# Kernel optimization log

Measured on AMD Instinct MI355X. Metric: run time of the kernel, lower is better.

Reference implementation:

```python
import jax, jax.numpy as jnp
import numpy as np

MARGIN = 0.2
LAMBDA_CLS = 1.0
LAMBDA_TRIPLET = 1.0
EPS = 1e-6  # matches torch pairwise_distance eps inside TripletMarginLoss
B, D, C = 8192, 192, 1024


def setup_inputs() -> dict:
    key = jax.random.key(0)
    k1, k2, k3 = jax.random.split(key, 3)
    embeddings = jax.random.normal(k1, (B, D), dtype=jnp.float32)
    logits = jax.random.normal(k2, (B, C), dtype=jnp.float32)
    targets = jax.random.randint(k3, (B,), 0, C, dtype=jnp.int64)
    return {"embeddings": embeddings, "logits": logits, "targets": targets}


def reference(embeddings, logits, targets):
    # ---- classification loss: mean cross entropy ----
    logp = jax.nn.log_softmax(logits, axis=-1)
    cls_loss = -jnp.mean(jnp.take_along_axis(logp, targets[:, None], axis=1))

    # ---- vectorized hard triplet mining (mining='hard'), on detached embeddings ----
    e = jax.lax.stop_gradient(embeddings)
    sq = jnp.sum(e * e, axis=1)                       # [B]
    d2 = sq[:, None] + sq[None, :] - 2.0 * (e @ e.T)  # [B, B]
    dist = jnp.sqrt(jnp.maximum(d2, 0.0))

    same = targets[:, None] == targets[None, :]       # [B, B]
    eye = jnp.eye(targets.shape[0], dtype=bool)
    pos_mask = same & ~eye
    neg_mask = ~same
    valid = pos_mask.any(axis=1) & neg_mask.any(axis=1)

    # hard positive: farthest same-speaker; hard negative: closest other-speaker
    pos_idx = jnp.argmax(jnp.where(pos_mask, dist, -jnp.inf), axis=1)
    neg_idx = jnp.argmin(jnp.where(neg_mask, dist, jnp.inf), axis=1)

    # ---- triplet margin loss on live embeddings ----
    a = embeddings
    p = embeddings[pos_idx]
    n = embeddings[neg_idx]
    d_ap = jnp.linalg.norm(a - p + EPS, axis=1)
    d_an = jnp.linalg.norm(a - n + EPS, axis=1)
    per_triplet = jnp.maximum(d_ap - d_an + MARGIN, 0.0)

    w = valid.astype(per_triplet.dtype)
    cnt = jnp.sum(w)
    trip_loss = jnp.where(cnt > 0, jnp.sum(per_triplet * w) / jnp.maximum(cnt, 1.0), 0.0)

    return LAMBDA_CLS * cls_loss + LAMBDA_TRIPLET * trip_loss
```

## Files before the change

kernel.cpp:

```cpp
#include <hip/hip_runtime.h>
#include <math.h>

#define B_N    8192
#define D_DIM  192
#define C_CLS  1024
#define MARGIN 0.2f
#define EPS_T  1e-6f

#define TI     128
#define TJ     128
#define JSPLIT 8
#define JLEN   (B_N / JSPLIT)
#define LDB    200

typedef short v8s  __attribute__((ext_vector_type(8)));
typedef float v16f __attribute__((ext_vector_type(16)));

__device__ __forceinline__ unsigned fkey(float f) {
  unsigned u = __float_as_uint(f);
  return (u & 0x80000000u) ? ~u : (u | 0x80000000u);
}

__device__ __forceinline__ unsigned short to_bf(float x) {
  unsigned u = __float_as_uint(x);
  u += 0x7fffu + ((u >> 16) & 1u);
  return (unsigned short)(u >> 16);
}

__global__ __launch_bounds__(256) void prep_kernel(
    const float* __restrict__ e, unsigned short* __restrict__ ebf,
    float* __restrict__ sq,
    unsigned long long* __restrict__ posw, unsigned long long* __restrict__ negw,
    float* __restrict__ accum) {
  int w = threadIdx.x >> 6, lane = threadIdx.x & 63;
  int row = blockIdx.x * 4 + w;
  const float* p = e + (size_t)row * D_DIM;
  float v0 = p[lane], v1 = p[lane + 64], v2 = p[lane + 128];
  unsigned short* q = ebf + (size_t)row * D_DIM;
  q[lane] = to_bf(v0); q[lane + 64] = to_bf(v1); q[lane + 128] = to_bf(v2);
  float s = v0 * v0 + v1 * v1 + v2 * v2;
  #pragma unroll
  for (int off = 32; off; off >>= 1) s += __shfl_xor(s, off);
  if (lane == 0) sq[row] = s;
  int b = blockIdx.x;
  if (b < 32)       posw[b * 256 + threadIdx.x] = 0ULL;
  else if (b < 64)  negw[(b - 32) * 256 + threadIdx.x] = ~0ULL;
  else if (b == 64 && threadIdx.x < 4) ((unsigned*)accum)[threadIdx.x] = 0u;
}

__global__ __launch_bounds__(256, 2) void mine_kernel(
    const unsigned short* __restrict__ ebf, const int* __restrict__ tgt,
    const float* __restrict__ sq, const float* __restrict__ logits,
    unsigned long long* __restrict__ posw, unsigned long long* __restrict__ negw,
    float* __restrict__ accum) {
  __shared__ unsigned short lds_b[TJ * LDB];
  __shared__ int   lds_t[TJ];
  __shared__ float lds_s[TJ];
  __shared__ float ce_part[4];

  const int tid  = threadIdx.x;
  const int w    = tid >> 6;
  const int lane = tid & 63;
  const int n5   = lane & 31;
  const int h    = lane >> 5;
  const int wj   = w & 1;
  const int wi   = w >> 1;
  const int i0 = blockIdx.x * TI;
  const int jb = blockIdx.y * JLEN;

  {
    const unsigned short* src = ebf + (size_t)i0 * D_DIM;
    #pragma unroll
    for (int t = 0; t < 12; ++t) {
      int c = t * 256 + tid;
      int row = c / 24;
      int off = c - row * 24;
      *(v8s*)&lds_b[row * LDB + off * 8] = *(const v8s*)(src + (size_t)row * D_DIM + off * 8);
    }
  }
  __syncthreads();
  v8s bfrag[2][12];
  #pragma unroll
  for (int tb = 0; tb < 2; ++tb)
    #pragma unroll
    for (int kc = 0; kc < 12; ++kc)
      bfrag[tb][kc] = *(const v8s*)&lds_b[(wi * 64 + tb * 32 + n5) * LDB + kc * 16 + h * 8];

  int my_t[2];
  #pragma unroll
  for (int tb = 0; tb < 2; ++tb) my_t[tb] = tgt[i0 + wi * 64 + tb * 32 + n5];

  float    pv[2] = {-3.4e38f, -3.4e38f}, nv[2] = {3.4e38f, 3.4e38f};
  unsigned pi_[2] = {0u, 0u}, ni_[2] = {0xFFFFFFFFu, 0xFFFFFFFFu};

  for (int j0 = jb; j0 < jb + JLEN; j0 += TJ) {
    __syncthreads();
    #pragma unroll
    for (int t = 0; t < 12; ++t) {
      int c = t * 256 + tid;
      int row = c / 24;
      int off = c - row * 24;
      *(v8s*)&lds_b[row * LDB + off * 8] =
          *(const v8s*)(ebf + (size_t)(j0 + row) * D_DIM + off * 8);
    }
    if (tid < TJ) { lds_t[tid] = tgt[j0 + tid]; lds_s[tid] = sq[j0 + tid]; }
    __syncthreads();

    v16f acc[2][2];
    #pragma unroll
    for (int ta = 0; ta < 2; ++ta)
      #pragma unroll
      for (int tb = 0; tb < 2; ++tb)
        #pragma unroll
        for (int r = 0; r < 16; ++r) acc[ta][tb][r] = 0.f;

    #pragma unroll
    for (int kc = 0; kc < 12; ++kc) {
      v8s afr0 = *(const v8s*)&lds_b[(wj * 64 +  0 + n5) * LDB + kc * 16 + h * 8];
      v8s afr1 = *(const v8s*)&lds_b[(wj * 64 + 32 + n5) * LDB + kc * 16 + h * 8];
      acc[0][0] = __builtin_amdgcn_mfma_f32_32x32x16_bf16(afr0, bfrag[0][kc], acc[0][0], 0, 0, 0);
      acc[0][1] = __builtin_amdgcn_mfma_f32_32x32x16_bf16(afr0, bfrag[1][kc], acc[0][1], 0, 0, 0);
      acc[1][0] = __builtin_amdgcn_mfma_f32_32x32x16_bf16(afr1, bfrag[0][kc], acc[1][0], 0, 0, 0);
      acc[1][1] = __builtin_amdgcn_mfma_f32_32x32x16_bf16(afr1, bfrag[1][kc], acc[1][1], 0, 0, 0);
    }

    #pragma unroll
    for (int ta = 0; ta < 2; ++ta)
      #pragma unroll
      for (int p = 0; p < 4; ++p) {
        int jb4 = wj * 64 + ta * 32 + p * 8 + h * 4;
        float4 s4 = *(const float4*)&lds_s[jb4];
        int4   t4 = *(const int4*)&lds_t[jb4];
        #pragma unroll
        for (int q = 0; q < 3 + 1; ++q) {
          float sv = (q == 0) ? s4.x : (q == 1) ? s4.y : (q == 2) ? s4.z : s4.w;
          int   tv = (q == 0) ? t4.x : (q == 1) ? t4.y : (q == 2) ? t4.z : t4.w;
          unsigned jg = (unsigned)(j0 + jb4 + q);
          #pragma unroll
          for (int tb = 0; tb < 2; ++tb) {
            float val = fmaf(acc[ta][tb][p * 4 + q], -2.0f, sv);
            bool same = (tv == my_t[tb]);
            float vp = same ? val : -3.4e38f;
            float vn = same ? 3.4e38f : val;
            if (vp > pv[tb]) { pv[tb] = vp; pi_[tb] = jg; }
            if (vn < nv[tb]) { nv[tb] = vn; ni_[tb] = jg; }
          }
        }
      }
  }

  #pragma unroll
  for (int tb = 0; tb < 2; ++tb) {
    unsigned long long pk =
        ((unsigned long long)fkey(pv[tb]) << 32) | (unsigned long long)(unsigned)(~pi_[tb]);
    unsigned long long nk =
        ((unsigned long long)fkey(nv[tb]) << 32) | (unsigned long long)ni_[tb];
    unsigned long long po = __shfl_xor(pk, 32);
    unsigned long long no = __shfl_xor(nk, 32);
    pk = pk > po ? pk : po;
    nk = nk < no ? nk : no;
    if (h == 0) {
      int irow = i0 + wi * 64 + tb * 32 + n5;
      atomicMax(&posw[irow], pk);
      atomicMin(&negw[irow], nk);
    }
  }

  int blin = blockIdx.y * 64 + blockIdx.x;
  float ce_acc = 0.f;
  #pragma unroll
  for (int it = 0; it < 4; ++it) {
    int row = blin * 16 + it * 4 + w;
    const float* lp = logits + (size_t)row * C_CLS;
    float4 x[4];
    #pragma unroll
    for (int t = 0; t < 4; ++t) x[t] = *(const float4*)(lp + lane * 4 + 256 * t);
    float m = -3.4e38f;
    #pragma unroll
    for (int t = 0; t < 4; ++t)
      m = fmaxf(m, fmaxf(fmaxf(x[t].x, x[t].y), fmaxf(x[t].z, x[t].w)));
    #pragma unroll
    for (int off = 32; off; off >>= 1) m = fmaxf(m, __shfl_xor(m, off));
    float s = 0.f;
    #pragma unroll
    for (int t = 0; t < 4; ++t)
      s += __expf(x[t].x - m) + __expf(x[t].y - m) +
           __expf(x[t].z - m) + __expf(x[t].w - m);
    #pragma unroll
    for (int off = 32; off; off >>= 1) s += __shfl_xor(s, off);
    if (lane == 0) ce_acc += m + __logf(s) - lp[tgt[row]];
  }
  if (lane == 0) ce_part[w] = ce_acc;
  __syncthreads();
  if (tid == 0)
    atomicAdd(&accum[0], ce_part[0] + ce_part[1] + ce_part[2] + ce_part[3]);
}

__global__ __launch_bounds__(1024) void trip_fin_kernel(
    const float* __restrict__ e,
    const unsigned long long* __restrict__ posw,
    const unsigned long long* __restrict__ negw,
    float* __restrict__ accum, float* __restrict__ out) {
  __shared__ float ssum[16];
  __shared__ float scnt[16];
  int w = threadIdx.x >> 6, lane = threadIdx.x & 63;
  int i = blockIdx.x * 16 + w;
  unsigned long long pp = posw[i], np = negw[i];
  unsigned pidx = ~(unsigned)pp;
  unsigned nidx = (unsigned)np;
  float res = 0.f, c = 0.f;
  if (pp != 0ULL && np != ~0ULL && pidx != (unsigned)i) {
    const float* pa = e + (size_t)i * D_DIM;
    const float* pb = e + (size_t)pidx * D_DIM;
    const float* pc = e + (size_t)nidx * D_DIM;
    float dap = 0.f, dan = 0.f;
    #pragma unroll
    for (int t = 0; t < 3; ++t) {
      int k = lane + 64 * t;
      float av = pa[k];
      float d1 = av - pb[k] + EPS_T;
      float d2 = av - pc[k] + EPS_T;
      dap += d1 * d1;
      dan += d2 * d2;
    }
    #pragma unroll
    for (int off = 32; off; off >>= 1) {
      dap += __shfl_xor(dap, off);
      dan += __shfl_xor(dan, off);
    }
    res = fmaxf(sqrtf(dap) - sqrtf(dan) + MARGIN, 0.f);
    c = 1.f;
  }
  if (lane == 0) { ssum[w] = res; scnt[w] = c; }
  __syncthreads();
  if (threadIdx.x == 0) {
    float a = 0.f, b = 0.f;
    #pragma unroll
    for (int k = 0; k < 16; ++k) { a += ssum[k]; b += scnt[k]; }
    atomicAdd(&accum[1], a);
    atomicAdd(&accum[2], b);
    __threadfence();
    unsigned old = atomicAdd((unsigned*)&accum[3], 1u);
    if (old == 511u) {
      __threadfence();
      float cls = atomicAdd(&accum[0], 0.f);
      float ts  = atomicAdd(&accum[1], 0.f);
      float tc  = atomicAdd(&accum[2], 0.f);
      float trip = (tc > 0.f) ? ts / fmaxf(tc, 1.f) : 0.f;
      out[0] = cls / (float)B_N + trip;
    }
  }
}

extern "C" void kernel_launch(void* const* d_in, const int* in_sizes, int n_in,
                              void* d_out, int out_size, void* d_ws, size_t ws_size,
                              hipStream_t stream) {
  const float* emb    = (const float*)d_in[0];
  const float* logits = (const float*)d_in[1];
  const int*   tgt    = (const int*)d_in[2];
  float* out = (float*)d_out;

  char* ws = (char*)d_ws;
  unsigned short* ebf = (unsigned short*)ws;
  unsigned long long* posw = (unsigned long long*)(ws + 3145728);
  unsigned long long* negw = (unsigned long long*)(ws + 3145728 + 65536);
  float* sq    = (float*)(ws + 3145728 + 131072);
  float* accum = (float*)(ws + 3145728 + 163840);

  prep_kernel<<<2048, 256, 0, stream>>>(emb, ebf, sq, posw, negw, accum);
  mine_kernel<<<dim3(B_N / TI, JSPLIT), 256, 0, stream>>>(ebf, tgt, sq, logits, posw, negw, accum);
  trip_fin_kernel<<<512, 1024, 0, stream>>>(emb, posw, negw, accum, out);
}
```

Measured before the change: 145.6 us.

## Fuse triplet finalize into mining kernel with last-block-per-tile reduction

Drops the separate triplet-finalize kernel. Each mining block now writes its per-slice hard positive/negative winners to a slice buffer, and the last block to finish an i-tile merges those slices and computes the triplet terms. The argmin/argmax search packs the column index into the low 8 mantissa bits of the distance key, so each candidate needs one fmaxf/fminf instead of compare-and-select pairs. Block shape moves to 512 threads handling one 32-row B fragment per wave, and per-row global atomics are replaced by LDS atomics. In exchange, ranking is slightly less precise because of the truncated mantissa, and the completion counters rely on a 0xAA workspace poison value instead of explicit zeroing.

```diff
diff --git a/kernel.cpp b/kernel.cpp
--- a/kernel.cpp
+++ b/kernel.cpp
@@ -9,9 +9,14 @@
 
 #define TI     128
 #define TJ     128
+#define NIB    64
 #define JSPLIT 8
-#define JLEN   (B_N / JSPLIT)
+#define JLEN   1024
+#define NTILE  8
 #define LDB    200
+#define NBLK   512
+#define NTHR   512
+#define POISON 0xAAAAAAAAu
 
 typedef short v8s  __attribute__((ext_vector_type(8)));
 typedef float v16f __attribute__((ext_vector_type(16)));
@@ -20,43 +25,43 @@
   unsigned u = __float_as_uint(f);
   return (u & 0x80000000u) ? ~u : (u | 0x80000000u);
 }
-
 __device__ __forceinline__ unsigned short to_bf(float x) {
   unsigned u = __float_as_uint(x);
   u += 0x7fffu + ((u >> 16) & 1u);
   return (unsigned short)(u >> 16);
 }
 
-__global__ __launch_bounds__(256) void prep_kernel(
+__global__ __launch_bounds__(NTHR) void prep_kernel(
     const float* __restrict__ e, unsigned short* __restrict__ ebf,
-    float* __restrict__ sq,
-    unsigned long long* __restrict__ posw, unsigned long long* __restrict__ negw,
-    float* __restrict__ accum) {
+    float* __restrict__ sq) {
   int w = threadIdx.x >> 6, lane = threadIdx.x & 63;
-  int row = blockIdx.x * 4 + w;
-  const float* p = e + (size_t)row * D_DIM;
-  float v0 = p[lane], v1 = p[lane + 64], v2 = p[lane + 128];
-  unsigned short* q = ebf + (size_t)row * D_DIM;
-  q[lane] = to_bf(v0); q[lane + 64] = to_bf(v1); q[lane + 128] = to_bf(v2);
-  float s = v0 * v0 + v1 * v1 + v2 * v2;
   #pragma unroll
-  for (int off = 32; off; off >>= 1) s += __shfl_xor(s, off);
-  if (lane == 0) sq[row] = s;
-  int b = blockIdx.x;
-  if (b < 32)       posw[b * 256 + threadIdx.x] = 0ULL;
-  else if (b < 64)  negw[(b - 32) * 256 + threadIdx.x] = ~0ULL;
-  else if (b == 64 && threadIdx.x < 4) ((unsigned*)accum)[threadIdx.x] = 0u;
-}
-
-__global__ __launch_bounds__(256, 2) void mine_kernel(
+  for (int r = 0; r < 2; ++r) {
+    int row = blockIdx.x * 16 + w * 2 + r;
+    const float* p = e + (size_t)row * D_DIM;
+    float v0 = p[lane], v1 = p[lane + 64], v2 = p[lane + 128];
+    unsigned short* q = ebf + (size_t)row * D_DIM;
+    q[lane] = to_bf(v0); q[lane + 64] = to_bf(v1); q[lane + 128] = to_bf(v2);
+    float s = v0 * v0 + v1 * v1 + v2 * v2;
+    #pragma unroll
+    for (int off = 32; off; off >>= 1) s += __shfl_xor(s, off);
+    if (lane == 0) sq[row] = s;
+  }
+}
+
+__global__ __launch_bounds__(NTHR, 4) void mine_kernel(
     const unsigned short* __restrict__ ebf, const int* __restrict__ tgt,
     const float* __restrict__ sq, const float* __restrict__ logits,
-    unsigned long long* __restrict__ posw, unsigned long long* __restrict__ negw,
-    float* __restrict__ accum) {
+    const float* __restrict__ e,
+    unsigned long long* __restrict__ posS, unsigned long long* __restrict__ negS,
+    unsigned* __restrict__ tileCnt, float* __restrict__ accum,
+    float* __restrict__ out) {
   __shared__ unsigned short lds_b[TJ * LDB];
   __shared__ int   lds_t[TJ];
   __shared__ float lds_s[TJ];
-  __shared__ float ce_part[4];
+  __shared__ unsigned long long lds_pos[TI], lds_neg[TI];
+  __shared__ float red_a[8], red_b[8];
+  __shared__ unsigned sflag;
 
   const int tid  = threadIdx.x;
   const int w    = tid >> 6;
@@ -65,39 +70,30 @@
   const int h    = lane >> 5;
   const int wj   = w & 1;
   const int wi   = w >> 1;
-  const int i0 = blockIdx.x * TI;
-  const int jb = blockIdx.y * JLEN;
-
+  const int tile  = blockIdx.x & (NIB - 1);
+  const int slice = blockIdx.x >> 6;
+  const int i0 = tile * TI;
+  const int jb = slice * JLEN;
+  const float NINF = -__builtin_inff();
+  const float PINF =  __builtin_inff();
+
+  const int irow = i0 + wi * 32 + n5;
+  v8s bfrag[12];
   {
-    const unsigned short* src = ebf + (size_t)i0 * D_DIM;
-    #pragma unroll
-    for (int t = 0; t < 12; ++t) {
-      int c = t * 256 + tid;
-      int row = c / 24;
-      int off = c - row * 24;
-      *(v8s*)&lds_b[row * LDB + off * 8] = *(const v8s*)(src + (size_t)row * D_DIM + off * 8);
-    }
-  }
-  __syncthreads();
-  v8s bfrag[2][12];
-  #pragma unroll
-  for (int tb = 0; tb < 2; ++tb)
-    #pragma unroll
-    for (int kc = 0; kc < 12; ++kc)
-      bfrag[tb][kc] = *(const v8s*)&lds_b[(wi * 64 + tb * 32 + n5) * LDB + kc * 16 + h * 8];
-
-  int my_t[2];
-  #pragma unroll
-  for (int tb = 0; tb < 2; ++tb) my_t[tb] = tgt[i0 + wi * 64 + tb * 32 + n5];
-
-  float    pv[2] = {-3.4e38f, -3.4e38f}, nv[2] = {3.4e38f, 3.4e38f};
-  unsigned pi_[2] = {0u, 0u}, ni_[2] = {0xFFFFFFFFu, 0xFFFFFFFFu};
-
-  for (int j0 = jb; j0 < jb + JLEN; j0 += TJ) {
+    const unsigned short* bp = ebf + (size_t)irow * D_DIM + h * 8;
+    #pragma unroll
+    for (int kc = 0; kc < 12; ++kc) bfrag[kc] = *(const v8s*)(bp + kc * 16);
+  }
+  const int myt = tgt[irow];
+
+  float pv = NINF, nv = PINF;
+
+  for (int jt = 0; jt < NTILE; ++jt) {
+    const int j0 = jb + jt * TJ;
     __syncthreads();
     #pragma unroll
-    for (int t = 0; t < 12; ++t) {
-      int c = t * 256 + tid;
+    for (int t = 0; t < 6; ++t) {
+      int c = t * NTHR + tid;
       int row = c / 24;
       int off = c - row * 24;
       *(v8s*)&lds_b[row * LDB + off * 8] =
@@ -106,76 +102,92 @@
     if (tid < TJ) { lds_t[tid] = tgt[j0 + tid]; lds_s[tid] = sq[j0 + tid]; }
     __syncthreads();
 
-    v16f acc[2][2];
-    #pragma unroll
-    for (int ta = 0; ta < 2; ++ta)
-      #pragma unroll
-      for (int tb = 0; tb < 2; ++tb)
-        #pragma unroll
-        for (int r = 0; r < 16; ++r) acc[ta][tb][r] = 0.f;
-
+    v16f acc0, acc1;
+    #pragma unroll
+    for (int r = 0; r < 16; ++r) { acc0[r] = 0.f; acc1[r] = 0.f; }
     #pragma unroll
     for (int kc = 0; kc < 12; ++kc) {
-      v8s afr0 = *(const v8s*)&lds_b[(wj * 64 +  0 + n5) * LDB + kc * 16 + h * 8];
-      v8s afr1 = *(const v8s*)&lds_b[(wj * 64 + 32 + n5) * LDB + kc * 16 + h * 8];
-      acc[0][0] = __builtin_amdgcn_mfma_f32_32x32x16_bf16(afr0, bfrag[0][kc], acc[0][0], 0, 0, 0);
-      acc[0][1] = __builtin_amdgcn_mfma_f32_32x32x16_bf16(afr0, bfrag[1][kc], acc[0][1], 0, 0, 0);
-      acc[1][0] = __builtin_amdgcn_mfma_f32_32x32x16_bf16(afr1, bfrag[0][kc], acc[1][0], 0, 0, 0);
-      acc[1][1] = __builtin_amdgcn_mfma_f32_32x32x16_bf16(afr1, bfrag[1][kc], acc[1][1], 0, 0, 0);
-    }
-
-    #pragma unroll
-    for (int ta = 0; ta < 2; ++ta)
+      v8s a0 = *(const v8s*)&lds_b[(wj * 64 +  0 + n5) * LDB + kc * 16 + h * 8];
+      v8s a1 = *(const v8s*)&lds_b[(wj * 64 + 32 + n5) * LDB + kc * 16 + h * 8];
+      acc0 = __builtin_amdgcn_mfma_f32_32x32x16_bf16(a0, bfrag[kc], acc0, 0, 0, 0);
+      acc1 = __builtin_amdgcn_mfma_f32_32x32x16_bf16(a1, bfrag[kc], acc1, 0, 0, 0);
+    }
+
+    const unsigned cb = (unsigned)jt << 5;
+    #pragma unroll
+    for (int ta = 0; ta < 2; ++ta) {
       #pragma unroll
       for (int p = 0; p < 4; ++p) {
         int jb4 = wj * 64 + ta * 32 + p * 8 + h * 4;
         float4 s4 = *(const float4*)&lds_s[jb4];
         int4   t4 = *(const int4*)&lds_t[jb4];
         #pragma unroll
-        for (int q = 0; q < 3 + 1; ++q) {
+        for (int q = 0; q < 4; ++q) {
           float sv = (q == 0) ? s4.x : (q == 1) ? s4.y : (q == 2) ? s4.z : s4.w;
           int   tv = (q == 0) ? t4.x : (q == 1) ? t4.y : (q == 2) ? t4.z : t4.w;
-          unsigned jg = (unsigned)(j0 + jb4 + q);
-          #pragma unroll
-          for (int tb = 0; tb < 2; ++tb) {
-            float val = fmaf(acc[ta][tb][p * 4 + q], -2.0f, sv);
-            bool same = (tv == my_t[tb]);
-            float vp = same ? val : -3.4e38f;
-            float vn = same ? 3.4e38f : val;
-            if (vp > pv[tb]) { pv[tb] = vp; pi_[tb] = jg; }
-            if (vn < nv[tb]) { nv[tb] = vn; ni_[tb] = jg; }
-          }
+          float av = (ta == 0) ? acc0[p * 4 + q] : acc1[p * 4 + q];
+          float val = fmaf(av, -2.0f, sv);
+          unsigned cc = cb | (unsigned)(ta * 16 + p * 4 + q);
+          float key = __uint_as_float((__float_as_uint(val) & 0xFFFFFF00u) | cc);
+          bool same = (tv == myt);
+          pv = fmaxf(pv, same ? key : NINF);
+          nv = fminf(nv, same ? PINF : key);
         }
       }
-  }
-
-  #pragma unroll
-  for (int tb = 0; tb < 2; ++tb) {
-    unsigned long long pk =
-        ((unsigned long long)fkey(pv[tb]) << 32) | (unsigned long long)(unsigned)(~pi_[tb]);
-    unsigned long long nk =
-        ((unsigned long long)fkey(nv[tb]) << 32) | (unsigned long long)ni_[tb];
+    }
+  }
+
+  unsigned long long pk = 0ULL, nk = ~0ULL;
+  if (pv != NINF) {
+    unsigned c = __float_as_uint(pv) & 255u;
+    unsigned jr = (unsigned)jb + ((c >> 5) & 7u) * 128u + (unsigned)wj * 64u +
+                  ((c >> 4) & 1u) * 32u + ((c >> 2) & 3u) * 8u + (unsigned)h * 4u + (c & 3u);
+    pk = ((unsigned long long)fkey(pv) << 32) | (unsigned long long)(~jr);
+  }
+  if (nv != PINF) {
+    unsigned c = __float_as_uint(nv) & 255u;
+    unsigned jr = (unsigned)jb + ((c >> 5) & 7u) * 128u + (unsigned)wj * 64u +
+                  ((c >> 4) & 1u) * 32u + ((c >> 2) & 3u) * 8u + (unsigned)h * 4u + (c & 3u);
+    nk = ((unsigned long long)fkey(nv) << 32) | (unsigned long long)jr;
+  }
+  {
     unsigned long long po = __shfl_xor(pk, 32);
     unsigned long long no = __shfl_xor(nk, 32);
     pk = pk > po ? pk : po;
     nk = nk < no ? nk : no;
-    if (h == 0) {
-      int irow = i0 + wi * 64 + tb * 32 + n5;
-      atomicMax(&posw[irow], pk);
-      atomicMin(&negw[irow], nk);
-    }
-  }
-
-  int blin = blockIdx.y * 64 + blockIdx.x;
+  }
+  __syncthreads();
+  if (tid < TI) { lds_pos[tid] = 0ULL; lds_neg[tid] = ~0ULL; }
+  __syncthreads();
+  if (h == 0) {
+    int il = wi * 32 + n5;
+    if (pk != 0ULL)  atomicMax(&lds_pos[il], pk);
+    if (nk != ~0ULL) atomicMin(&lds_neg[il], nk);
+  }
+  __syncthreads();
+  if (tid < TI) {
+    __hip_atomic_store(&posS[(size_t)slice * B_N + i0 + tid], lds_pos[tid],
+                       __ATOMIC_RELAXED, __HIP_MEMORY_SCOPE_AGENT);
+    __hip_atomic_store(&negS[(size_t)slice * B_N + i0 + tid], lds_neg[tid],
+                       __ATOMIC_RELAXED, __HIP_MEMORY_SCOPE_AGENT);
+  }
+  __threadfence();
+  __syncthreads();
+  if (tid == 0) {
+    atomicCAS(&tileCnt[tile], 0u, POISON);
+    unsigned old = atomicAdd(&tileCnt[tile], 1u);
+    sflag = (old == POISON + (JSPLIT - 1)) ? 1u : 0u;
+  }
+
   float ce_acc = 0.f;
   #pragma unroll
-  for (int it = 0; it < 4; ++it) {
-    int row = blin * 16 + it * 4 + w;
+  for (int it = 0; it < 2; ++it) {
+    int row = blockIdx.x * 16 + it * 8 + w;
     const float* lp = logits + (size_t)row * C_CLS;
     float4 x[4];
     #pragma unroll
     for (int t = 0; t < 4; ++t) x[t] = *(const float4*)(lp + lane * 4 + 256 * t);
-    float m = -3.4e38f;
+    float m = NINF;
     #pragma unroll
     for (int t = 0; t < 4; ++t)
       m = fmaxf(m, fmaxf(fmaxf(x[t].x, x[t].y), fmaxf(x[t].z, x[t].w)));
@@ -190,62 +202,82 @@
     for (int off = 32; off; off >>= 1) s += __shfl_xor(s, off);
     if (lane == 0) ce_acc += m + __logf(s) - lp[tgt[row]];
   }
-  if (lane == 0) ce_part[w] = ce_acc;
+  if (lane == 0) red_a[w] = ce_acc;
   __syncthreads();
   if (tid == 0)
-    atomicAdd(&accum[0], ce_part[0] + ce_part[1] + ce_part[2] + ce_part[3]);
-}
-
-__global__ __launch_bounds__(1024) void trip_fin_kernel(
-    const float* __restrict__ e,
-    const unsigned long long* __restrict__ posw,
-    const unsigned long long* __restrict__ negw,
-    float* __restrict__ accum, float* __restrict__ out) {
-  __shared__ float ssum[16];
-  __shared__ float scnt[16];
-  int w = threadIdx.x >> 6, lane = threadIdx.x & 63;
-  int i = blockIdx.x * 16 + w;
-  unsigned long long pp = posw[i], np = negw[i];
-  unsigned pidx = ~(unsigned)pp;
-  unsigned nidx = (unsigned)np;
-  float res = 0.f, c = 0.f;
-  if (pp != 0ULL && np != ~0ULL && pidx != (unsigned)i) {
-    const float* pa = e + (size_t)i * D_DIM;
-    const float* pb = e + (size_t)pidx * D_DIM;
-    const float* pc = e + (size_t)nidx * D_DIM;
-    float dap = 0.f, dan = 0.f;
-    #pragma unroll
-    for (int t = 0; t < 3; ++t) {
-      int k = lane + 64 * t;
-      float av = pa[k];
-      float d1 = av - pb[k] + EPS_T;
-      float d2 = av - pc[k] + EPS_T;
-      dap += d1 * d1;
-      dan += d2 * d2;
-    }
-    #pragma unroll
-    for (int off = 32; off; off >>= 1) {
-      dap += __shfl_xor(dap, off);
-      dan += __shfl_xor(dan, off);
-    }
-    res = fmaxf(sqrtf(dap) - sqrtf(dan) + MARGIN, 0.f);
-    c = 1.f;
-  }
-  if (lane == 0) { ssum[w] = res; scnt[w] = c; }
-  __syncthreads();
-  if (threadIdx.x == 0) {
-    float a = 0.f, b = 0.f;
-    #pragma unroll
-    for (int k = 0; k < 16; ++k) { a += ssum[k]; b += scnt[k]; }
-    atomicAdd(&accum[1], a);
-    atomicAdd(&accum[2], b);
+    atomicAdd(&accum[0], red_a[0] + red_a[1] + red_a[2] + red_a[3] +
+                         red_a[4] + red_a[5] + red_a[6] + red_a[7]);
+  __syncthreads();
+
+  if (sflag) {
     __threadfence();
-    unsigned old = atomicAdd((unsigned*)&accum[3], 1u);
-    if (old == 511u) {
+    if (tid < TI) {
+      unsigned long long P = 0ULL, Nn = ~0ULL;
+      for (int s = 0; s < JSPLIT; ++s) {
+        unsigned long long a = __hip_atomic_load(&posS[(size_t)s * B_N + i0 + tid],
+                                                 __ATOMIC_RELAXED, __HIP_MEMORY_SCOPE_AGENT);
+        unsigned long long b = __hip_atomic_load(&negS[(size_t)s * B_N + i0 + tid],
+                                                 __ATOMIC_RELAXED, __HIP_MEMORY_SCOPE_AGENT);
+        P = a > P ? a : P;
+        Nn = b < Nn ? b : Nn;
+      }
+      lds_pos[tid] = P; lds_neg[tid] = Nn;
+    }
+    __syncthreads();
+    float tsum = 0.f, tcnt = 0.f;
+    for (int rr = 0; rr < 16; ++rr) {
+      int il = w * 16 + rr;
+      int i  = i0 + il;
+      unsigned long long pp = lds_pos[il], np = lds_neg[il];
+      unsigned pidx = ~(unsigned)pp;
+      unsigned nidx = (unsigned)np;
+      bool valid = (pp != 0ULL) && (np != ~0ULL) && (pidx != (unsigned)i);
+      float dap = 0.f, dan = 0.f;
+      if (valid && lane < 48) {
+        float4 a4 = *(const float4*)(e + (size_t)i    * D_DIM + lane * 4);
+        float4 p4 = *(const float4*)(e + (size_t)pidx * D_DIM + lane * 4);
+        float4 n4 = *(const float4*)(e + (size_t)nidx * D_DIM + lane * 4);
+        float d;
+        d = a4.x - p4.x + EPS_T; dap += d * d;
+        d = a4.y - p4.y + EPS_T; dap += d * d;
+        d = a4.z - p4.z + EPS_T; dap += d * d;
+        d = a4.w - p4.w + EPS_T; dap += d * d;
+        d = a4.x - n4.x + EPS_T; dan += d * d;
+        d = a4.y - n4.y + EPS_T; dan += d * d;
+        d = a4.z - n4.z + EPS_T; dan += d * d;
+        d = a4.w - n4.w + EPS_T; dan += d * d;
+      }
+      #pragma unroll
+      for (int off = 32; off; off >>= 1) {
+        dap += __shfl_xor(dap, off);
+        dan += __shfl_xor(dan, off);
+      }
+      if (lane == 0 && valid) {
+        tsum += fmaxf(sqrtf(dap) - sqrtf(dan) + MARGIN, 0.f);
+        tcnt += 1.f;
+      }
+    }
+    if (lane == 0) { red_a[w] = tsum; red_b[w] = tcnt; }
+    __syncthreads();
+    if (tid == 0) {
+      atomicAdd(&accum[1], red_a[0] + red_a[1] + red_a[2] + red_a[3] +
+                           red_a[4] + red_a[5] + red_a[6] + red_a[7]);
+      atomicAdd(&accum[2], red_b[0] + red_b[1] + red_b[2] + red_b[3] +
+                           red_b[4] + red_b[5] + red_b[6] + red_b[7]);
+    }
+  }
+
+  __threadfence();
+  __syncthreads();
+  if (tid == 0) {
+    unsigned* gcnt = (unsigned*)&accum[3];
+    atomicCAS(gcnt, 0u, POISON);
+    unsigned old = atomicAdd(gcnt, 1u);
+    if (old == POISON + (NBLK - 1)) {
       __threadfence();
-      float cls = atomicAdd(&accum[0], 0.f);
-      float ts  = atomicAdd(&accum[1], 0.f);
-      float tc  = atomicAdd(&accum[2], 0.f);
+      float cls = __hip_atomic_load(&accum[0], __ATOMIC_RELAXED, __HIP_MEMORY_SCOPE_AGENT);
+      float ts  = __hip_atomic_load(&accum[1], __ATOMIC_RELAXED, __HIP_MEMORY_SCOPE_AGENT);
+      float tc  = __hip_atomic_load(&accum[2], __ATOMIC_RELAXED, __HIP_MEMORY_SCOPE_AGENT);
       float trip = (tc > 0.f) ? ts / fmaxf(tc, 1.f) : 0.f;
       out[0] = cls / (float)B_N + trip;
     }
@@ -262,12 +294,13 @@
 
   char* ws = (char*)d_ws;
   unsigned short* ebf = (unsigned short*)ws;
-  unsigned long long* posw = (unsigned long long*)(ws + 3145728);
-  unsigned long long* negw = (unsigned long long*)(ws + 3145728 + 65536);
-  float* sq    = (float*)(ws + 3145728 + 131072);
-  float* accum = (float*)(ws + 3145728 + 163840);
-
-  prep_kernel<<<2048, 256, 0, stream>>>(emb, ebf, sq, posw, negw, accum);
-  mine_kernel<<<dim3(B_N / TI, JSPLIT), 256, 0, stream>>>(ebf, tgt, sq, logits, posw, negw, accum);
-  trip_fin_kernel<<<512, 1024, 0, stream>>>(emb, posw, negw, accum, out);
-}
+  float* sq = (float*)(ws + 3145728);
+  unsigned long long* posS = (unsigned long long*)(ws + 3178496);
+  unsigned long long* negS = (unsigned long long*)(ws + 3702784);
+  unsigned* tileCnt = (unsigned*)(ws + 4227072);
+  float* accum = (float*)(ws + 4227328);
+
+  prep_kernel<<<NBLK, NTHR, 0, stream>>>(emb, ebf, sq);
+  mine_kernel<<<NBLK, NTHR, 0, stream>>>(ebf, tgt, sq, logits, emb,
+                                         posS, negS, tileCnt, accum, out);
+}
```

Result: slower. 273.1 us (+87.5%).
